# Kernel tuning notes

Hardware: AMD Instinct MI355X
Metric: run time of the kernel (lower is better)

Reference implementation:

```python
import jax, jax.numpy as jnp
import numpy as np

N_NODES = 25000
N_EDGES = 300000
N_GRAPHS = 256
EMB_DIM = 92
HID = 256
EDGE_F = 4


def _lin(key, fan_in, fan_out):
    kw, kb = jax.random.split(key)
    s = 1.0 / np.sqrt(fan_in)
    W = jax.random.uniform(kw, (fan_in, fan_out), jnp.float32, -s, s)
    b = jax.random.uniform(kb, (fan_out,), jnp.float32, -s, s)
    return W, b


def setup_inputs() -> dict:
    key = jax.random.key(0)
    ks = jax.random.split(key, 32)
    x_atoms = jax.random.randint(ks[0], (N_NODES,), 0, 119)
    edge_index = jax.random.randint(ks[1], (2, N_EDGES), 0, N_NODES)
    edge_attr = jax.random.normal(ks[2], (N_EDGES, EDGE_F), jnp.float32)
    batch = jnp.sort(jax.random.randint(ks[3], (N_NODES,), 0, N_GRAPHS))
    emb = jax.random.normal(ks[4], (119, EMB_DIM), jnp.float32)
    emb = emb.at[0].set(0.0)  # padding_idx=0
    # layer 0: in=92, out=256
    ew1_0, eb1_0 = _lin(ks[5], EDGE_F, EMB_DIM)
    ew2_0, eb2_0 = _lin(ks[6], EMB_DIM, EMB_DIM)
    nw_0, nb_0 = _lin(ks[7], EMB_DIM, HID)
    # layers 1..3 stacked: in=out=256
    ew1, eb1, ew2, eb2, nw, nb = [], [], [], [], [], []
    for i in range(3):
        a, b = _lin(ks[8 + 3 * i], EDGE_F, HID)
        c, d = _lin(ks[9 + 3 * i], HID, HID)
        e, f = _lin(ks[10 + 3 * i], HID, HID)
        ew1.append(a); eb1.append(b); ew2.append(c); eb2.append(d); nw.append(e); nb.append(f)
    ew1 = jnp.stack(ew1); eb1 = jnp.stack(eb1); ew2 = jnp.stack(ew2)
    eb2 = jnp.stack(eb2); nw = jnp.stack(nw); nb = jnp.stack(nb)
    rw1, rb1 = _lin(ks[20], HID, HID)
    rw2, rb2 = _lin(ks[21], HID, HID // 2)
    rw3, rb3 = _lin(ks[22], HID // 2, 1)
    return dict(x_atoms=x_atoms, edge_index=edge_index, edge_attr=edge_attr, batch=batch,
                emb=emb, ew1_0=ew1_0, eb1_0=eb1_0, ew2_0=ew2_0, eb2_0=eb2_0, nw_0=nw_0, nb_0=nb_0,
                ew1=ew1, eb1=eb1, ew2=ew2, eb2=eb2, nw=nw, nb=nb,
                rw1=rw1, rb1=rb1, rw2=rw2, rb2=rb2, rw3=rw3, rb3=rb3)


def _conv(x, src, dst, edge_attr, ew1, eb1, ew2, eb2, nw, nb):
    # edge MLP: Linear -> Softplus -> Linear
    ee = jax.nn.softplus(edge_attr @ ew1 + eb1) @ ew2 + eb2  # [E, C]
    msg = ee * x[src]                                        # gather + multiply
    agg = jax.ops.segment_sum(msg, dst, num_segments=x.shape[0])  # scatter-add
    return jax.nn.softplus(agg @ nw + nb)


def reference(x_atoms, edge_index, edge_attr, batch, emb,
              ew1_0, eb1_0, ew2_0, eb2_0, nw_0, nb_0,
              ew1, eb1, ew2, eb2, nw, nb,
              rw1, rb1, rw2, rb2, rw3, rb3):
    src, dst = edge_index[0], edge_index[1]  # PyG: x_j = x[src], aggregate at dst
    x = emb[x_atoms]  # [N, 92]
    x = _conv(x, src, dst, edge_attr, ew1_0, eb1_0, ew2_0, eb2_0, nw_0, nb_0)
    for i in range(3):
        x = _conv(x, src, dst, edge_attr, ew1[i], eb1[i], ew2[i], eb2[i], nw[i], nb[i])
    # global mean pool
    sums = jax.ops.segment_sum(x, batch, num_segments=N_GRAPHS)
    cnts = jax.ops.segment_sum(jnp.ones((x.shape[0],), x.dtype), batch, num_segments=N_GRAPHS)
    g = sums / jnp.maximum(cnts, 1.0)[:, None]  # [G, 256]
    h = jax.nn.softplus(g @ rw1 + rb1)          # dropout is identity in eval mode
    h = jax.nn.softplus(h @ rw2 + rb2)
    out = (h @ rw3 + rb3).squeeze(-1)           # [G]
    return out
```

## Files before the change

### kernel.cpp

```cpp
#include <hip/hip_runtime.h>
#include <math.h>

#define N_NODES  25000
#define N_EDGES  300000
#define N_GRAPHS 256
#define EMB_DIM  92
#define HID      256

typedef short bf16x8 __attribute__((ext_vector_type(8)));
typedef float f32x4  __attribute__((ext_vector_type(4)));

__device__ __forceinline__ float softplusf(float x){
    return fmaxf(x, 0.0f) + __logf(1.0f + __expf(-fabsf(x)));
}
__device__ __forceinline__ unsigned short f2bf(float f){
    unsigned int u = __float_as_uint(f);
    unsigned int r = (u + 0x7FFFu + ((u >> 16) & 1u)) >> 16;
    return (unsigned short)r;
}
__device__ __forceinline__ unsigned short f2bf_trunc(float f){
    return (unsigned short)(__float_as_uint(f) >> 16);
}
__device__ __forceinline__ float bf2f(unsigned short b){
    return __uint_as_float(((unsigned int)b) << 16);
}
__device__ __forceinline__ void split_bf(float h, unsigned short& hi, unsigned short& lo){
    const unsigned int u = __float_as_uint(h);
    hi = (unsigned short)(u >> 16);
    const float r = h - __uint_as_float(u & 0xFFFF0000u);
    lo = (unsigned short)(__float_as_uint(r) >> 16);
}
__device__ __forceinline__ int xcd_window(int nwin){
    const int per = (nwin + 7) >> 3;
    const int win = (blockIdx.x & 7) * per + (blockIdx.x >> 3);
    return (win < nwin) ? win : -1;
}

__global__ void gather_emb_kernel(const int* __restrict__ atoms,
                                  const float* __restrict__ emb,
                                  float* __restrict__ x)
{
    const int n = blockIdx.x;
    const int c = threadIdx.x;
    if (c < EMB_DIM){
        const int a = atoms[n];
        x[(size_t)n*EMB_DIM + c] = emb[(size_t)a*EMB_DIM + c];
    }
}

__global__ __launch_bounds__(256) void hist_kernel(const int* __restrict__ dst, int* __restrict__ hist){
    const int e = blockIdx.x*256 + threadIdx.x;
    if (e < N_EDGES) atomicAdd(&hist[dst[e]], 1);
}

__global__ __launch_bounds__(1024) void scan_kernel(const int* __restrict__ hist, int* __restrict__ cursor){
    __shared__ int chunk[1024];
    const int t = threadIdx.x;
    const int base = t*25;
    int local[25];
    int s = 0;
    #pragma unroll
    for (int i=0;i<25;i++){
        const int idx = base+i;
        const int v = (idx < N_NODES) ? hist[idx] : 0;
        local[i] = s; s += v;
    }
    chunk[t] = s;
    __syncthreads();
    for (int off=1; off<1024; off<<=1){
        int v = (t >= off) ? chunk[t-off] : 0;
        __syncthreads();
        chunk[t] += v;
        __syncthreads();
    }
    const int pre = (t > 0) ? chunk[t-1] : 0;
    #pragma unroll
    for (int i=0;i<25;i++){
        const int idx = base+i;
        if (idx < N_NODES) cursor[idx] = pre + local[i];
    }
}

__global__ __launch_bounds__(256) void scatter_kernel(const int* __restrict__ src, const int* __restrict__ dst,
                                                      const float* __restrict__ ea,
                                                      int* __restrict__ cursor,
                                                      int* __restrict__ src_s, int* __restrict__ dst_s,
                                                      float* __restrict__ ea_s){
    const int e = blockIdx.x*256 + threadIdx.x;
    if (e < N_EDGES){
        const int d = dst[e];
        const int pos = atomicAdd(&cursor[d], 1);
        src_s[pos] = src[e];
        dst_s[pos] = d;
        const float4 a = *(const float4*)(ea + (size_t)e*4);
        *(float4*)(ea_s + (size_t)pos*4) = a;
    }
}

__global__ __launch_bounds__(256) void pack_w_kernel(const float* __restrict__ w,
                                                     unsigned short* __restrict__ whi,
                                                     unsigned short* __restrict__ wlo)
{
    const int f     = blockIdx.x;
    const int layer = f >> 7;
    const int rem   = f & 127;
    const int ntile = rem >> 3;
    const int k8    = rem & 7;
    for (int i = threadIdx.x; i < 512; i += 256){
        const int lane = i >> 3, j = i & 7;
        const int k = k8*32 + (lane >> 4)*8 + j;
        const int n = ntile*16 + (lane & 15);
        const float v = w[(size_t)layer*HID*HID + (size_t)k*HID + n];
        const unsigned short hb = f2bf(v);
        whi[(size_t)f*512 + i] = hb;
        wlo[(size_t)f*512 + i] = f2bf(v - bf2f(hb));
    }
}

__global__ __launch_bounds__(256) void pack_w_pad_kernel(const float* __restrict__ w,
                                                         int Kin, int Nin, int ldn,
                                                         unsigned short* __restrict__ whi,
                                                         unsigned short* __restrict__ wlo)
{
    const int f  = blockIdx.x;
    const int k8 = f % 3;
    const int ntile = f / 3;
    for (int i = threadIdx.x; i < 512; i += 256){
        const int lane = i >> 3, j = i & 7;
        const int k = k8*32 + (lane >> 4)*8 + j;
        const int n = ntile*16 + (lane & 15);
        float v = 0.0f;
        if (k < Kin && n < Nin) v = w[(size_t)k*ldn + n];
        const unsigned short hb = f2bf(v);
        whi[(size_t)f*512 + i] = hb;
        wlo[(size_t)f*512 + i] = f2bf(v - bf2f(hb));
    }
}

__global__ __launch_bounds__(256, 4) void edge_conv92_mfma_kernel(
    const int* __restrict__ src_s, const int* __restrict__ dst_s,
    const float* __restrict__ ea_s,
    const float* __restrict__ w1, const float* __restrict__ b1,
    const unsigned short* __restrict__ whi, const unsigned short* __restrict__ wlo,
    const float* __restrict__ b2,
    const float* __restrict__ x92, float* __restrict__ agg92)
{
    constexpr int C = EMB_DIM;
    constexpr int KP = 96;
    constexpr int LDA = 104;
    constexpr int EPB = 64;
    constexpr int NWIN = (N_EDGES + EPB - 1) / EPB;
    __shared__ unsigned short aHi[EPB][LDA];
    __shared__ float eaS[EPB][4];
    __shared__ int   srcS[EPB];
    __shared__ int   dstS[EPB];

    const int win = xcd_window(NWIN);
    if (win < 0) return;
    const int e0  = win * EPB;
    const int tid = threadIdx.x;

    {
        const int e = tid >> 2, comp = tid & 3;
        const int eid = min(e0 + e, N_EDGES-1);
        eaS[e][comp] = ea_s[(size_t)eid*4 + comp];
        if (tid < EPB){
            const int eid2 = min(e0 + tid, N_EDGES-1);
            srcS[tid] = src_s[eid2];
            dstS[tid] = dst_s[eid2];
        }
    }
    __syncthreads();

    for (int idx = tid; idx < EPB*KP; idx += 256){
        const int e = idx / KP, k = idx - e*KP;
        float h = 0.0f;
        if (k < C){
            const float4 a = *(const float4*)&eaS[e][0];
            h = softplusf(fmaf(a.x, w1[k], fmaf(a.y, w1[C+k],
                          fmaf(a.z, w1[2*C+k], fmaf(a.w, w1[3*C+k], b1[k])))));
        }
        const int row = (e>>5)*32 + ((e>>2)&1)*16 + ((e>>3)&3)*4 + (e&3);
        aHi[row][k] = f2bf_trunc(h);
    }
    __syncthreads();

    const int lane = tid & 63, wv = tid >> 6;
    const int quad = lane >> 4, fcol = lane & 15;
    const int mpair = wv >> 1;
    const int ngrp  = wv & 1;

    f32x4 acc[2][3];
    #pragma unroll
    for (int m=0;m<2;m++)
        #pragma unroll
        for (int t=0;t<3;t++)
            #pragma unroll
            for (int j=0;j<4;j++) acc[m][t][j] = 0.0f;

    for (int k8=0;k8<3;k8++){
        bf16x8 ah[2];
        #pragma unroll
        for (int m=0;m<2;m++)
            ah[m] = *(const bf16x8*)(&aHi[mpair*32 + m*16 + fcol][0] + k8*32 + quad*8);
        #pragma unroll
        for (int t=0;t<3;t++){
            const int fi = (ngrp*3 + t)*3 + k8;
            const bf16x8 bh = *(const bf16x8*)(whi + (size_t)fi*512 + lane*8);
            const bf16x8 bl = *(const bf16x8*)(wlo + (size_t)fi*512 + lane*8);
            #pragma unroll
            for (int m=0;m<2;m++){
                acc[m][t] = __builtin_amdgcn_mfma_f32_16x16x32_bf16(ah[m], bh, acc[m][t], 0, 0, 0);
                acc[m][t] = __builtin_amdgcn_mfma_f32_16x16x32_bf16(ah[m], bl, acc[m][t], 0, 0, 0);
            }
        }
    }

    int   ncol[3]; float bb[3];
    #pragma unroll
    for (int t=0;t<3;t++){
        ncol[t] = (ngrp*3 + t)*16 + fcol;
        bb[t] = (ncol[t] < C) ? b2[ncol[t]] : 0.0f;
    }

    const int ebase = mpair*32 + quad*8;
    float xv[8][3];
    #pragma unroll
    for (int j=0;j<8;j++){
        const int s = srcS[ebase + j];
        const bool valid = (e0 + ebase + j) < N_EDGES;
        #pragma unroll
        for (int t=0;t<3;t++)
            xv[j][t] = (valid && ncol[t] < C) ? x92[(size_t)s*C + ncol[t]] : 0.0f;
    }

    int dprev = dstS[ebase];
    float run[3] = {0.f,0.f,0.f};
    #pragma unroll
    for (int j=0;j<8;j++){
        const int d = dstS[ebase + j];
        if (d != dprev){
            #pragma unroll
            for (int t=0;t<3;t++){
                if (ncol[t] < C) atomicAdd(&agg92[(size_t)dprev*C + ncol[t]], run[t]);
                run[t] = 0.0f;
            }
            dprev = d;
        }
        #pragma unroll
        for (int t=0;t<3;t++)
            run[t] += (acc[j>>2][t][j&3] + bb[t]) * xv[j][t];
    }
    #pragma unroll
    for (int t=0;t<3;t++)
        if (ncol[t] < C) atomicAdd(&agg92[(size_t)dprev*C + ncol[t]], run[t]);
}

__global__ __launch_bounds__(256) void node_update92_mfma_kernel(
    const float* __restrict__ agg92,
    const unsigned short* __restrict__ whi, const unsigned short* __restrict__ wlo,
    const float* __restrict__ b, float* __restrict__ xout)
{
    constexpr int C = EMB_DIM;
    constexpr int KP = 96;
    constexpr int LDA = 104;
    __shared__ unsigned short aHi[16][LDA];
    __shared__ unsigned short aLo[16][LDA];

    const int n0  = blockIdx.x * 16;
    const int tid = threadIdx.x;

    for (int idx = tid; idx < 16*KP; idx += 256){
        const int i = idx / KP, k = idx - i*KP;
        const int node = n0 + i;
        float v = 0.0f;
        if (k < C && node < N_NODES) v = agg92[(size_t)node*C + k];
        unsigned short hb, lb;
        split_bf(v, hb, lb);
        aHi[i][k] = hb;
        aLo[i][k] = lb;
    }
    __syncthreads();

    const int lane = tid & 63, wv = tid >> 6;
    const int quad = lane >> 4, fcol = lane & 15;

    f32x4 acc[4];
    #pragma unroll
    for (int t=0;t<4;t++)
        #pragma unroll
        for (int j=0;j<4;j++) acc[t][j] = 0.0f;

    const unsigned short* aHrow = &aHi[fcol][0];
    const unsigned short* aLrow = &aLo[fcol][0];

    for (int k8=0;k8<3;k8++){
        const bf16x8 ah = *(const bf16x8*)(aHrow + k8*32 + quad*8);
        const bf16x8 al = *(const bf16x8*)(aLrow + k8*32 + quad*8);
        #pragma unroll
        for (int t=0;t<4;t++){
            const int fi = (wv*4 + t)*3 + k8;
            const bf16x8 bh = *(const bf16x8*)(whi + (size_t)fi*512 + lane*8);
            const bf16x8 bl = *(const bf16x8*)(wlo + (size_t)fi*512 + lane*8);
            acc[t] = __builtin_amdgcn_mfma_f32_16x16x32_bf16(ah, bh, acc[t], 0, 0, 0);
            acc[t] = __builtin_amdgcn_mfma_f32_16x16x32_bf16(ah, bl, acc[t], 0, 0, 0);
            acc[t] = __builtin_amdgcn_mfma_f32_16x16x32_bf16(al, bh, acc[t], 0, 0, 0);
        }
    }

    #pragma unroll
    for (int i=0;i<4;i++){
        const int node = n0 + quad*4 + i;
        if (node < N_NODES){
            #pragma unroll
            for (int t=0;t<4;t++){
                const int n = (wv*4 + t)*16 + fcol;
                xout[(size_t)node*HID + n] = softplusf(acc[t][i] + b[n]);
            }
        }
    }
}

__global__ __launch_bounds__(256, 4) void edge_conv256_mfma_kernel(
    const int* __restrict__ src_s, const int* __restrict__ dst_s,
    const float* __restrict__ ea_s,
    const float* __restrict__ w1, const float* __restrict__ b1,
    const unsigned short* __restrict__ whi, const unsigned short* __restrict__ wlo,
    const float* __restrict__ b2,
    const float* __restrict__ x, float* __restrict__ agg)
{
    constexpr int C = HID;
    constexpr int LDA = C + 8;
    constexpr int EPB = 64;
    constexpr int NWIN = (N_EDGES + EPB - 1) / EPB;
    __shared__ unsigned short aHi[EPB][LDA];
    __shared__ float eaS[EPB][4];
    __shared__ int   srcS[EPB];
    __shared__ int   dstS[EPB];

    const int win = xcd_window(NWIN);
    if (win < 0) return;
    const int e0  = win * EPB;
    const int tid = threadIdx.x;

    {
        const int e = tid >> 2, comp = tid & 3;
        const int eid = min(e0 + e, N_EDGES-1);
        eaS[e][comp] = ea_s[(size_t)eid*4 + comp];
        if (tid < EPB){
            const int eid2 = min(e0 + tid, N_EDGES-1);
            srcS[tid] = src_s[eid2];
            dstS[tid] = dst_s[eid2];
        }
    }
    __syncthreads();

    {
        const int k = tid;
        const float w10 = w1[k], w11 = w1[C+k], w12 = w1[2*C+k], w13 = w1[3*C+k];
        const float bk  = b1[k];
        #pragma unroll
        for (int e=0;e<EPB;e++){
            const float4 a = *(const float4*)&eaS[e][0];
            const float v = fmaf(a.x,w10,fmaf(a.y,w11,fmaf(a.z,w12,fmaf(a.w,w13,bk))));
            const int q = e >> 4, j = e & 15;
            aHi[(j>>2)*16 + q*4 + (j&3)][k] = f2bf_trunc(softplusf(v));
        }
    }
    __syncthreads();

    const int lane = tid & 63, wv = tid >> 6;
    const int quad = lane >> 4, fcol = lane & 15;

    f32x4 acc[4][4];
    #pragma unroll
    for (int m=0;m<4;m++)
        #pragma unroll
        for (int t=0;t<4;t++)
            #pragma unroll
            for (int j=0;j<4;j++) acc[m][t][j] = 0.0f;

    for (int k8=0;k8<8;k8++){
        bf16x8 ah[4];
        #pragma unroll
        for (int m=0;m<4;m++)
            ah[m] = *(const bf16x8*)(&aHi[m*16 + fcol][0] + k8*32 + quad*8);
        #pragma unroll
        for (int t=0;t<4;t++){
            const int fi = (wv*4 + t)*8 + k8;
            const bf16x8 bh = *(const bf16x8*)(whi + (size_t)fi*512 + lane*8);
            const bf16x8 bl = *(const bf16x8*)(wlo + (size_t)fi*512 + lane*8);
            #pragma unroll
            for (int m=0;m<4;m++){
                acc[m][t] = __builtin_amdgcn_mfma_f32_16x16x32_bf16(ah[m], bh, acc[m][t], 0, 0, 0);
                acc[m][t] = __builtin_amdgcn_mfma_f32_16x16x32_bf16(ah[m], bl, acc[m][t], 0, 0, 0);
            }
        }
    }

    float bb[4];
    #pragma unroll
    for (int t=0;t<4;t++) bb[t] = b2[(wv*4 + t)*16 + fcol];

    const int ebase = quad*16;
    int dprev = dstS[ebase];
    float run[4] = {0.f,0.f,0.f,0.f};
    #pragma unroll
    for (int jj=0; jj<16; jj+=4){
        float xv[4][4];
        #pragma unroll
        for (int j2=0;j2<4;j2++){
            const int j = jj + j2;
            const int s = srcS[ebase + j];
            const bool valid = (e0 + ebase + j) < N_EDGES;
            #pragma unroll
            for (int t=0;t<4;t++)
                xv[j2][t] = valid ? x[(size_t)s*C + (wv*4 + t)*16 + fcol] : 0.0f;
        }
        #pragma unroll
        for (int j2=0;j2<4;j2++){
            const int j = jj + j2;
            const int d = dstS[ebase + j];
            if (d != dprev){
                #pragma unroll
                for (int t=0;t<4;t++){
                    atomicAdd(&agg[(size_t)dprev*C + (wv*4 + t)*16 + fcol], run[t]);
                    run[t] = 0.0f;
                }
                dprev = d;
            }
            const int m = j >> 2, i = j & 3;
            #pragma unroll
            for (int t=0;t<4;t++)
                run[t] += (acc[m][t][i] + bb[t]) * xv[j2][t];
        }
    }
    #pragma unroll
    for (int t=0;t<4;t++)
        atomicAdd(&agg[(size_t)dprev*C + (wv*4 + t)*16 + fcol], run[t]);
}

__global__ __launch_bounds__(256) void node_update_mfma_kernel(
    const float* __restrict__ agg,
    const unsigned short* __restrict__ whi, const unsigned short* __restrict__ wlo,
    const float* __restrict__ b, float* __restrict__ xout)
{
    constexpr int C = HID;
    constexpr int LDA = C + 8;
    __shared__ unsigned short aHi[16][LDA];
    __shared__ unsigned short aLo[16][LDA];

    const int n0  = blockIdx.x * 16;
    const int tid = threadIdx.x;

    #pragma unroll
    for (int it=0; it<16; it++){
        const int node = n0 + it;
        const float v = (node < N_NODES) ? agg[(size_t)node*C + tid] : 0.0f;
        unsigned short hb, lb;
        split_bf(v, hb, lb);
        aHi[it][tid] = hb;
        aLo[it][tid] = lb;
    }
    __syncthreads();

    const int lane = tid & 63, wv = tid >> 6;
    const int quad = lane >> 4, fcol = lane & 15;

    f32x4 acc[4];
    #pragma unroll
    for (int t=0;t<4;t++)
        #pragma unroll
        for (int j=0;j<4;j++) acc[t][j] = 0.0f;

    const unsigned short* aHrow = &aHi[fcol][0];
    const unsigned short* aLrow = &aLo[fcol][0];

    for (int k8=0;k8<8;k8++){
        const bf16x8 ah = *(const bf16x8*)(aHrow + k8*32 + quad*8);
        const bf16x8 al = *(const bf16x8*)(aLrow + k8*32 + quad*8);
        #pragma unroll
        for (int t=0;t<4;t++){
            const int fi = (wv*4 + t)*8 + k8;
            const bf16x8 bh = *(const bf16x8*)(whi + (size_t)fi*512 + lane*8);
            const bf16x8 bl = *(const bf16x8*)(wlo + (size_t)fi*512 + lane*8);
            acc[t] = __builtin_amdgcn_mfma_f32_16x16x32_bf16(ah, bh, acc[t], 0, 0, 0);
            acc[t] = __builtin_amdgcn_mfma_f32_16x16x32_bf16(ah, bl, acc[t], 0, 0, 0);
            acc[t] = __builtin_amdgcn_mfma_f32_16x16x32_bf16(al, bh, acc[t], 0, 0, 0);
        }
    }

    #pragma unroll
    for (int i=0;i<4;i++){
        const int node = n0 + quad*4 + i;
        if (node < N_NODES){
            #pragma unroll
            for (int t=0;t<4;t++){
                const int n = (wv*4 + t)*16 + fcol;
                xout[(size_t)node*C + n] = softplusf(acc[t][i] + b[n]);
            }
        }
    }
}

__global__ __launch_bounds__(256) void pool_kernel(
    const float* __restrict__ x, const int* __restrict__ batch,
    float* __restrict__ sums, float* __restrict__ cnts)
{
    constexpr int NPB = 32;
    const int n0 = blockIdx.x * NPB;
    const int c  = threadIdx.x;
    int gprev = batch[n0];
    float run = 0.0f, crun = 0.0f;
    for (int i=0;i<NPB;i++){
        const int n = n0 + i;
        if (n >= N_NODES) break;
        const int g = batch[n];
        if (g != gprev){
            atomicAdd(&sums[(size_t)gprev*HID + c], run);
            if (c == 0) atomicAdd(&cnts[gprev], crun);
            run = 0.0f; crun = 0.0f; gprev = g;
        }
        run  += x[(size_t)n*HID + c];
        crun += 1.0f;
    }
    atomicAdd(&sums[(size_t)gprev*HID + c], run);
    if (c == 0) atomicAdd(&cnts[gprev], crun);
}

__global__ __launch_bounds__(256) void readout_kernel(
    const float* __restrict__ sums, const float* __restrict__ cnts,
    const float* __restrict__ rw1, const float* __restrict__ rb1,
    const float* __restrict__ rw2, const float* __restrict__ rb2,
    const float* __restrict__ rw3, const float* __restrict__ rb3,
    float* __restrict__ out)
{
    __shared__ float g[HID];
    __shared__ float h[HID];
    __shared__ float h2[HID/2];
    __shared__ float red[256];
    const int gi = blockIdx.x;
    const int t  = threadIdx.x;
    const float cnt = fmaxf(cnts[gi], 1.0f);
    g[t] = sums[(size_t)gi*HID + t] / cnt;
    __syncthreads();
    float acc = rb1[t];
    for (int k=0;k<HID;k++) acc = fmaf(g[k], rw1[(size_t)k*HID + t], acc);
    h[t] = softplusf(acc);
    __syncthreads();
    if (t < HID/2){
        float a2 = rb2[t];
        for (int k=0;k<HID;k++) a2 = fmaf(h[k], rw2[(size_t)k*(HID/2) + t], a2);
        h2[t] = softplusf(a2);
    }
    __syncthreads();
    red[t] = (t < HID/2) ? h2[t]*rw3[t] : 0.0f;
    __syncthreads();
    for (int s2=128; s2>0; s2>>=1){
        if (t < s2) red[t] += red[t+s2];
        __syncthreads();
    }
    if (t == 0) out[gi] = red[0] + rb3[0];
}

extern "C" void kernel_launch(void* const* d_in, const int* in_sizes, int n_in,
                              void* d_out, int out_size, void* d_ws, size_t ws_size,
                              hipStream_t stream)
{
    const int*   x_atoms = (const int*)d_in[0];
    const int*   eidx    = (const int*)d_in[1];
    const int*   src     = eidx;
    const int*   dst     = eidx + N_EDGES;
    const float* ea      = (const float*)d_in[2];
    const int*   batch   = (const int*)d_in[3];
    const float* emb     = (const float*)d_in[4];
    const float* ew1_0   = (const float*)d_in[5];
    const float* eb1_0   = (const float*)d_in[6];
    const float* ew2_0   = (const float*)d_in[7];
    const float* eb2_0   = (const float*)d_in[8];
    const float* nw_0    = (const float*)d_in[9];
    const float* nb_0    = (const float*)d_in[10];
    const float* ew1     = (const float*)d_in[11];
    const float* eb1     = (const float*)d_in[12];
    const float* ew2     = (const float*)d_in[13];
    const float* eb2     = (const float*)d_in[14];
    const float* nw      = (const float*)d_in[15];
    const float* nb      = (const float*)d_in[16];
    const float* rw1     = (const float*)d_in[17];
    const float* rb1     = (const float*)d_in[18];
    const float* rw2     = (const float*)d_in[19];
    const float* rb2     = (const float*)d_in[20];
    const float* rw3     = (const float*)d_in[21];
    const float* rb3     = (const float*)d_in[22];
    float* out = (float*)d_out;

    float* x    = (float*)d_ws;
    float* agg  = x   + (size_t)N_NODES*HID;
    float* sums = agg + (size_t)N_NODES*HID;
    float* cnts = sums + (size_t)N_GRAPHS*HID;
    unsigned short* whi  = (unsigned short*)(cnts + N_GRAPHS);
    unsigned short* wlo  = whi  + (size_t)3*128*512;
    unsigned short* nwhi = wlo  + (size_t)3*128*512;
    unsigned short* nwlo = nwhi + (size_t)3*128*512;
    unsigned short* w92hi  = nwlo  + (size_t)3*128*512;
    unsigned short* w92lo  = w92hi + (size_t)18*512;
    unsigned short* nw92hi = w92lo + (size_t)18*512;
    unsigned short* nw92lo = nw92hi + (size_t)48*512;
    float* ea_s = (float*)(nw92lo + (size_t)48*512);
    int* hist   = (int*)(ea_s + (size_t)N_EDGES*4);
    int* cursor = hist   + N_NODES;
    int* src_s  = cursor + N_NODES;
    int* dst_s  = src_s  + N_EDGES;

    hipMemsetAsync(hist, 0, N_NODES*sizeof(int), stream);
    hipLaunchKernelGGL(hist_kernel, dim3((N_EDGES+255)/256), dim3(256), 0, stream, dst, hist);
    hipLaunchKernelGGL(scan_kernel, dim3(1), dim3(1024), 0, stream, hist, cursor);
    hipLaunchKernelGGL(scatter_kernel, dim3((N_EDGES+255)/256), dim3(256), 0, stream,
                       src, dst, ea, cursor, src_s, dst_s, ea_s);

    hipLaunchKernelGGL(pack_w_kernel, dim3(384), dim3(256), 0, stream, ew2, whi, wlo);
    hipLaunchKernelGGL(pack_w_kernel, dim3(384), dim3(256), 0, stream, nw, nwhi, nwlo);
    hipLaunchKernelGGL(pack_w_pad_kernel, dim3(18), dim3(256), 0, stream, ew2_0, EMB_DIM, EMB_DIM, EMB_DIM, w92hi, w92lo);
    hipLaunchKernelGGL(pack_w_pad_kernel, dim3(48), dim3(256), 0, stream, nw_0, EMB_DIM, HID, HID, nw92hi, nw92lo);

    const int NWIN64 = (N_EDGES + 63) / 64;

    hipLaunchKernelGGL(gather_emb_kernel, dim3(N_NODES), dim3(128), 0, stream, x_atoms, emb, x);
    hipMemsetAsync(agg, 0, (size_t)N_NODES*EMB_DIM*sizeof(float), stream);
    hipLaunchKernelGGL(edge_conv92_mfma_kernel, dim3((NWIN64+7)/8*8), dim3(256), 0, stream,
                       src_s, dst_s, ea_s, ew1_0, eb1_0, w92hi, w92lo, eb2_0, x, agg);
    hipLaunchKernelGGL(node_update92_mfma_kernel, dim3((N_NODES+15)/16), dim3(256), 0, stream,
                       agg, nw92hi, nw92lo, nb_0, x);

    for (int i=0;i<3;i++){
        hipMemsetAsync(agg, 0, (size_t)N_NODES*HID*sizeof(float), stream);
        hipLaunchKernelGGL(edge_conv256_mfma_kernel, dim3((NWIN64+7)/8*8), dim3(256), 0, stream,
                           src_s, dst_s, ea_s,
                           ew1 + (size_t)i*4*HID, eb1 + (size_t)i*HID,
                           whi + (size_t)i*128*512, wlo + (size_t)i*128*512,
                           eb2 + (size_t)i*HID,
                           x, agg);
        hipLaunchKernelGGL(node_update_mfma_kernel, dim3((N_NODES+15)/16), dim3(256), 0, stream,
                           agg, nwhi + (size_t)i*128*512, nwlo + (size_t)i*128*512,
                           nb + (size_t)i*HID, x);
    }

    hipMemsetAsync(sums, 0, ((size_t)N_GRAPHS*HID + N_GRAPHS)*sizeof(float), stream);
    hipLaunchKernelGGL(pool_kernel, dim3((N_NODES+31)/32), dim3(256), 0, stream, x, batch, sums, cnts);
    hipLaunchKernelGGL(readout_kernel, dim3(N_GRAPHS), dim3(256), 0, stream,
                       sums, cnts, rw1, rb1, rw2, rb2, rw3, rb3, out);
}
```

Before: 753.0 us.

## Split edge conv across 8 waves and fuse agg zeroing into node update

```diff
diff --git a/kernel.cpp b/kernel.cpp
--- a/kernel.cpp
+++ b/kernel.cpp
@@ -321,7 +321,7 @@
     }
 }
 
-__global__ __launch_bounds__(256, 4) void edge_conv256_mfma_kernel(
+__global__ __launch_bounds__(512, 6) void edge_conv256_mfma_kernel(
     const int* __restrict__ src_s, const int* __restrict__ dst_s,
     const float* __restrict__ ea_s,
     const float* __restrict__ w1, const float* __restrict__ b1,
@@ -343,24 +343,27 @@
     const int e0  = win * EPB;
     const int tid = threadIdx.x;
 
-    {
+    if (tid < 256){
         const int e = tid >> 2, comp = tid & 3;
         const int eid = min(e0 + e, N_EDGES-1);
         eaS[e][comp] = ea_s[(size_t)eid*4 + comp];
-        if (tid < EPB){
-            const int eid2 = min(e0 + tid, N_EDGES-1);
-            srcS[tid] = src_s[eid2];
-            dstS[tid] = dst_s[eid2];
-        }
+    } else if (tid < 320){
+        const int e = tid - 256;
+        srcS[e] = src_s[min(e0 + e, N_EDGES-1)];
+    } else if (tid < 384){
+        const int e = tid - 320;
+        dstS[e] = dst_s[min(e0 + e, N_EDGES-1)];
     }
     __syncthreads();
 
     {
-        const int k = tid;
+        const int k = tid & 255;
+        const int g = tid >> 8;
         const float w10 = w1[k], w11 = w1[C+k], w12 = w1[2*C+k], w13 = w1[3*C+k];
         const float bk  = b1[k];
         #pragma unroll
-        for (int e=0;e<EPB;e++){
+        for (int ii=0; ii<32; ii++){
+            const int e = g*32 + ii;
             const float4 a = *(const float4*)&eaS[e][0];
             const float v = fmaf(a.x,w10,fmaf(a.y,w11,fmaf(a.z,w12,fmaf(a.w,w13,bk))));
             const int q = e >> 4, j = e & 15;
@@ -372,11 +375,11 @@
     const int lane = tid & 63, wv = tid >> 6;
     const int quad = lane >> 4, fcol = lane & 15;
 
-    f32x4 acc[4][4];
+    f32x4 acc[4][2];
     #pragma unroll
     for (int m=0;m<4;m++)
         #pragma unroll
-        for (int t=0;t<4;t++)
+        for (int t=0;t<2;t++)
             #pragma unroll
             for (int j=0;j<4;j++) acc[m][t][j] = 0.0f;
 
@@ -386,8 +389,8 @@
         for (int m=0;m<4;m++)
             ah[m] = *(const bf16x8*)(&aHi[m*16 + fcol][0] + k8*32 + quad*8);
         #pragma unroll
-        for (int t=0;t<4;t++){
-            const int fi = (wv*4 + t)*8 + k8;
+        for (int t=0;t<2;t++){
+            const int fi = (wv*2 + t)*8 + k8;
             const bf16x8 bh = *(const bf16x8*)(whi + (size_t)fi*512 + lane*8);
             const bf16x8 bl = *(const bf16x8*)(wlo + (size_t)fi*512 + lane*8);
             #pragma unroll
@@ -398,52 +401,47 @@
         }
     }
 
-    float bb[4];
-    #pragma unroll
-    for (int t=0;t<4;t++) bb[t] = b2[(wv*4 + t)*16 + fcol];
+    float bb[2];
+    #pragma unroll
+    for (int t=0;t<2;t++) bb[t] = b2[(wv*2 + t)*16 + fcol];
 
     const int ebase = quad*16;
+    float xv[16][2];
+    #pragma unroll
+    for (int j=0;j<16;j++){
+        const int s = srcS[ebase + j];
+        const bool valid = (e0 + ebase + j) < N_EDGES;
+        #pragma unroll
+        for (int t=0;t<2;t++)
+            xv[j][t] = valid ? x[(size_t)s*C + (wv*2 + t)*16 + fcol] : 0.0f;
+    }
+
     int dprev = dstS[ebase];
-    float run[4] = {0.f,0.f,0.f,0.f};
-    #pragma unroll
-    for (int jj=0; jj<16; jj+=4){
-        float xv[4][4];
-        #pragma unroll
-        for (int j2=0;j2<4;j2++){
-            const int j = jj + j2;
-            const int s = srcS[ebase + j];
-            const bool valid = (e0 + ebase + j) < N_EDGES;
-            #pragma unroll
-            for (int t=0;t<4;t++)
-                xv[j2][t] = valid ? x[(size_t)s*C + (wv*4 + t)*16 + fcol] : 0.0f;
-        }
-        #pragma unroll
-        for (int j2=0;j2<4;j2++){
-            const int j = jj + j2;
-            const int d = dstS[ebase + j];
-            if (d != dprev){
-                #pragma unroll
-                for (int t=0;t<4;t++){
-                    atomicAdd(&agg[(size_t)dprev*C + (wv*4 + t)*16 + fcol], run[t]);
-                    run[t] = 0.0f;
-                }
-                dprev = d;
+    float run[2] = {0.f,0.f};
+    #pragma unroll
+    for (int j=0;j<16;j++){
+        const int d = dstS[ebase + j];
+        if (d != dprev){
+            #pragma unroll
+            for (int t=0;t<2;t++){
+                atomicAdd(&agg[(size_t)dprev*C + (wv*2 + t)*16 + fcol], run[t]);
+                run[t] = 0.0f;
             }
-            const int m = j >> 2, i = j & 3;
-            #pragma unroll
-            for (int t=0;t<4;t++)
-                run[t] += (acc[m][t][i] + bb[t]) * xv[j2][t];
-        }
-    }
-    #pragma unroll
-    for (int t=0;t<4;t++)
-        atomicAdd(&agg[(size_t)dprev*C + (wv*4 + t)*16 + fcol], run[t]);
+            dprev = d;
+        }
+        #pragma unroll
+        for (int t=0;t<2;t++)
+            run[t] += (acc[j>>2][t][j&3] + bb[t]) * xv[j][t];
+    }
+    #pragma unroll
+    for (int t=0;t<2;t++)
+        atomicAdd(&agg[(size_t)dprev*C + (wv*2 + t)*16 + fcol], run[t]);
 }
 
 __global__ __launch_bounds__(256) void node_update_mfma_kernel(
-    const float* __restrict__ agg,
+    float* __restrict__ agg,
     const unsigned short* __restrict__ whi, const unsigned short* __restrict__ wlo,
-    const float* __restrict__ b, float* __restrict__ xout)
+    const float* __restrict__ b, float* __restrict__ xout, int zero_agg)
 {
     constexpr int C = HID;
     constexpr int LDA = C + 8;
@@ -456,7 +454,11 @@
     #pragma unroll
     for (int it=0; it<16; it++){
         const int node = n0 + it;
-        const float v = (node < N_NODES) ? agg[(size_t)node*C + tid] : 0.0f;
+        float v = 0.0f;
+        if (node < N_NODES){
+            v = agg[(size_t)node*C + tid];
+            if (zero_agg) agg[(size_t)node*C + tid] = 0.0f;
+        }
         unsigned short hb, lb;
         split_bf(v, hb, lb);
         aHi[it][tid] = hb;
@@ -632,9 +634,10 @@
     hipLaunchKernelGGL(node_update92_mfma_kernel, dim3((N_NODES+15)/16), dim3(256), 0, stream,
                        agg, nw92hi, nw92lo, nb_0, x);
 
+    hipMemsetAsync(agg, 0, (size_t)N_NODES*HID*sizeof(float), stream);
+
     for (int i=0;i<3;i++){
-        hipMemsetAsync(agg, 0, (size_t)N_NODES*HID*sizeof(float), stream);
-        hipLaunchKernelGGL(edge_conv256_mfma_kernel, dim3((NWIN64+7)/8*8), dim3(256), 0, stream,
+        hipLaunchKernelGGL(edge_conv256_mfma_kernel, dim3((NWIN64+7)/8*8), dim3(512), 0, stream,
                            src_s, dst_s, ea_s,
                            ew1 + (size_t)i*4*HID, eb1 + (size_t)i*HID,
                            whi + (size_t)i*128*512, wlo + (size_t)i*128*512,
@@ -642,7 +645,7 @@
                            x, agg);
         hipLaunchKernelGGL(node_update_mfma_kernel, dim3((N_NODES+15)/16), dim3(256), 0, stream,
                            agg, nwhi + (size_t)i*128*512, nwlo + (size_t)i*128*512,
-                           nb + (size_t)i*HID, x);
+                           nb + (size_t)i*HID, x, (i < 2) ? 1 : 0);
     }
 
     hipMemsetAsync(sums, 0, ((size_t)N_GRAPHS*HID + N_GRAPHS)*sizeof(float), stream);
```

Result: faster. 703.1 us (-6.6%).
